# Kernel optimization log

Measured on AMD Instinct MI355X. Metric: run time of the kernel, lower is better.

## Reference

```python
import jax, jax.numpy as jnp
import numpy as np

# sizes / constants (mirroring the source module's constants)
M, T_SOL, NX, NY = 12, 64, 256, 256
N_TIMES, NOUT = 50, 256
LX, LY_TARGET = 60.0, 75.0
C_CU_TARGET, C_NI_TARGET = 0.001, 0.0001
T_MAX = 200.0
SIGMA, H, DH = 0.25, 4, 8


def setup_inputs() -> dict:
    key = jax.random.key(0)
    ks = jax.random.split(key, 7)
    u = jax.random.uniform(ks[0], (M, 3), dtype=jnp.float32)
    # rows: (Ly in [30,120], c_Cu in [0,0.0029], c_Ni in [0,0.0018])
    params = jnp.stack([30.0 + 90.0 * u[:, 0], 0.0029 * u[:, 1], 0.0018 * u[:, 2]], axis=1)
    c1_src = jax.random.uniform(ks[1], (M, T_SOL, NX, NY), dtype=jnp.float32) * 0.003
    c2_src = jax.random.uniform(ks[2], (M, T_SOL, NX, NY), dtype=jnp.float32) * 0.002
    Wq = jax.random.normal(ks[3], (H * DH, 3), dtype=jnp.float32) * 0.5
    bq = jax.random.normal(ks[4], (H * DH,), dtype=jnp.float32) * 0.1
    Wk = jax.random.normal(ks[5], (H * DH, 3), dtype=jnp.float32) * 0.5
    bk = jax.random.normal(ks[6], (H * DH,), dtype=jnp.float32) * 0.1
    return {"params": params, "c1_src": c1_src, "c2_src": c2_src,
            "Wq": Wq, "bq": bq, "Wk": Wk, "bk": bk}


def _bilinear_resample(xs, ys, vals, xq, yq):
    """RegularGridInterpolator(linear, fill_value=0) on grid (xs[NX], ys[NY]).
    vals: [T, NX, NY]; query is the outer-product grid xq[PX] x yq[PY].
    Separable bilinear -> [T, PX, PY]."""
    ix = jnp.clip(jnp.searchsorted(xs, xq, side='right') - 1, 0, xs.shape[0] - 2)
    tx = (xq - xs[ix]) / (xs[ix + 1] - xs[ix])
    vx = vals[:, ix, :] * (1.0 - tx)[None, :, None] + vals[:, ix + 1, :] * tx[None, :, None]
    iy = jnp.clip(jnp.searchsorted(ys, yq, side='right') - 1, 0, ys.shape[0] - 2)
    ty = (yq - ys[iy]) / (ys[iy + 1] - ys[iy])
    out = vx[:, :, iy] * (1.0 - ty)[None, None, :] + vx[:, :, iy + 1] * ty[None, None, :]
    inb = ((xq >= xs[0]) & (xq <= xs[-1]))[:, None] & ((yq >= ys[0]) & (yq <= ys[-1]))[None, :]
    return jnp.where(inb[None], out, jnp.float32(0.0))


def _forward(params, c1_src, c2_src, Wq, bq, Wk, bk):
    lys, c_cus, c_nis = params[:, 0], params[:, 1], params[:, 2]
    ly_n = (lys - 30.0) / 90.0
    ccu_n = c_cus / 0.0029
    cni_n = c_nis / 0.0018
    p = jnp.stack([ly_n, ccu_n, cni_n], axis=1)                      # [M,3]
    t = jnp.array([[(LY_TARGET - 30.0) / 90.0,
                    C_CU_TARGET / 0.0029,
                    C_NI_TARGET / 0.0018]], dtype=params.dtype)       # [1,3]
    Q = (t @ Wq.T + bq).reshape(1, H, DH)
    K = (p @ Wk.T + bk).reshape(-1, H, DH)
    attn = jnp.einsum('nhd,mhd->nmh', K, Q) / (DH ** 0.5)            # [M,1,H]
    attn_w = jax.nn.softmax(attn, axis=0).mean(axis=2)[:, 0]         # [M]
    dist2 = (((ly_n - t[0, 0]) / SIGMA) ** 2
             + ((ccu_n - t[0, 1]) / SIGMA) ** 2
             + ((cni_n - t[0, 2]) / SIGMA) ** 2)
    sw = jnp.exp(-dist2 / 2.0)
    sw = sw / sw.sum()
    w = attn_w * sw
    w = w / w.sum()                                                  # [M]

    # grids: source x shared; per-solution y grid rescaled to [0, LY_TARGET]
    xs = jnp.linspace(0.0, LX, NX)
    ys_scaled = (jnp.linspace(0.0, 1.0, NY)[None, :] * lys[:, None]) * (LY_TARGET / lys)[:, None]  # [M,NY]
    xq = jnp.linspace(0.0, LX, NOUT)
    yq = jnp.linspace(0.0, LY_TARGET, NOUT)

    times = jnp.linspace(0.0, min(T_MAX, T_MAX), N_TIMES)
    tidx = jnp.clip((times / T_MAX * T_SOL).astype(jnp.int32), 0, T_SOL - 1)  # [T]
    c1_sel = c1_src[:, tidx]                                          # [M,T,NX,NY]
    c2_sel = c2_src[:, tidx]

    res1, res2 = jax.vmap(
        lambda ys, v1, v2: (_bilinear_resample(xs, ys, v1, xq, yq),
                            _bilinear_resample(xs, ys, v2, xq, yq))
    )(ys_scaled, c1_sel, c2_sel)                                      # each [M,T,NOUT,NOUT]

    c1 = jnp.einsum('m,mtij->tij', w, res1)
    c2 = jnp.einsum('m,mtij->tij', w, res2)
    c1 = c1.at[:, :, 0].set(C_CU_TARGET)
    c2 = c2.at[:, :, -1].set(C_NI_TARGET)
    return jnp.stack([c1, c2])                                        # [2,T,NOUT,NOUT]


def reference(params, c1_src, c2_src, Wq, bq, Wk, bk):
    return _forward(params, c1_src, c2_src, Wq, bq, Wk, bk)
```

## Files before the change

kernel.cpp:

```cpp
#include <hip/hip_runtime.h>

#define MM    12
#define TSOL  64
#define NXX   256
#define NYY   256
#define NTT   50
#define NOUTT 256

__device__ float g_c[MM * NOUTT];
__device__ float g_w[MM];
__device__ float g_w255[MM];

__global__ __launch_bounds__(256) void ai_setup_kernel(
    const float* __restrict__ params,
    const float* __restrict__ Wq, const float* __restrict__ bq,
    const float* __restrict__ Wk, const float* __restrict__ bk)
{
    const int k = threadIdx.x;
    const int m = blockIdx.x;

    __shared__ float s_attn[MM][4];
    __shared__ float s_sw[MM];
    __shared__ float s_wm;
    __shared__ float s_ys[NYY];

    if (k < MM) {
        float ly = params[k * 3 + 0];
        float p0 = (ly - 30.0f) / 90.0f;
        float p1 = params[k * 3 + 1] / 0.0029f;
        float p2 = params[k * 3 + 2] / 0.0018f;
        const float t0 = 0.5f;
        const float t1 = 0.001f / 0.0029f;
        const float t2 = 0.0001f / 0.0018f;
        for (int h = 0; h < 4; ++h) {
            float acc = 0.0f;
            for (int d = 0; d < 8; ++d) {
                int o = h * 8 + d;
                float q  = t0 * Wq[o * 3 + 0] + t1 * Wq[o * 3 + 1] + t2 * Wq[o * 3 + 2] + bq[o];
                float kv = p0 * Wk[o * 3 + 0] + p1 * Wk[o * 3 + 1] + p2 * Wk[o * 3 + 2] + bk[o];
                acc += kv * q;
            }
            s_attn[k][h] = acc * 0.35355339059327373f;
        }
        float d0 = (p0 - t0) / 0.25f;
        float d1 = (p1 - t1) / 0.25f;
        float d2 = (p2 - t2) / 0.25f;
        s_sw[k] = expf(-(d0 * d0 + d1 * d1 + d2 * d2) * 0.5f);
    }
    __syncthreads();

    if (k == 0) {
        float aw[MM];
        for (int j = 0; j < MM; ++j) aw[j] = 0.0f;
        for (int h = 0; h < 4; ++h) {
            float mx = s_attn[0][h];
            for (int j = 1; j < MM; ++j) mx = fmaxf(mx, s_attn[j][h]);
            float e[MM]; float sum = 0.0f;
            for (int j = 0; j < MM; ++j) { e[j] = expf(s_attn[j][h] - mx); sum += e[j]; }
            for (int j = 0; j < MM; ++j) aw[j] += e[j] / sum;
        }
        float swsum = 0.0f;
        for (int j = 0; j < MM; ++j) swsum += s_sw[j];
        float wj[MM]; float wsum = 0.0f;
        for (int j = 0; j < MM; ++j) {
            wj[j] = (aw[j] * 0.25f) * (s_sw[j] / swsum);
            wsum += wj[j];
        }
        s_wm = wj[m] / wsum;
    }

    {
        float ly  = params[m * 3 + 0];
        float inv = 75.0f / ly;
        float l01 = (float)k * (1.0f / 255.0f);
        s_ys[k] = (l01 * ly) * inv;
    }
    __syncthreads();

    float w  = s_wm;
    float yq = (float)k * (75.0f / 255.0f);
    int l = 0, r = NYY;
    while (l < r) { int mid = (l + r) >> 1; if (s_ys[mid] <= yq) l = mid + 1; else r = mid; }
    int iy = l - 1;
    iy = iy < 0 ? 0 : (iy > NYY - 2 ? NYY - 2 : iy);
    float ty  = (yq - s_ys[iy]) / (s_ys[iy + 1] - s_ys[iy]);
    bool  inb = (yq >= s_ys[0]) && (yq <= s_ys[NYY - 1]);
    float a = inb ? w * (1.0f - ty) : 0.0f;
    float b = inb ? w * ty          : 0.0f;
    bool sel = (iy == k);
    g_c[m * NOUTT + k] = sel ? b : -a;
    if (k == 0)   g_w[m]    = w;
    if (k == 255) g_w255[m] = inb ? w : 0.0f;
}

__global__ __launch_bounds__(256) void ai_resample_kernel(
    const float* __restrict__ c1, const float* __restrict__ c2,
    float* __restrict__ out)
{
    __shared__ float s_c[MM * NOUTT];

    const int tid  = threadIdx.x;
    const int lane = tid & 63;
    const int wv   = tid >> 6;
    const int t    = blockIdx.y;
    const int i    = blockIdx.x * 4 + wv;
    int tsrc = (t * TSOL) / (NTT - 1);
    if (tsrc > TSOL - 1) tsrc = TSOL - 1;
    const int k0   = lane * 4;
    const bool l63 = (lane == 63);

#pragma unroll
    for (int c = 0; c < 3; ++c) {
        const float* gp = g_c + c * 1024 + wv * 256 + lane * 4;
        float*       lp = s_c + c * 1024 + wv * 256;
        __builtin_amdgcn_global_load_lds(
            (const __attribute__((address_space(1))) void*)gp,
            (__attribute__((address_space(3))) void*)lp, 16, 0, 0);
    }

    float wmv[MM], w2v[MM];
#pragma unroll
    for (int m = 0; m < MM; ++m) { wmv[m] = g_w[m]; w2v[m] = g_w255[m]; }

    const size_t rowoff = (size_t)tsrc * (NXX * NYY) + (size_t)i * NYY + (size_t)k0;

    float4 st[MM];
#pragma unroll
    for (int m = 0; m < MM; ++m)
        st[m] = *(const float4*)(c1 + (size_t)m * (TSOL * NXX * NYY) + rowoff);

    __syncthreads();

    float4 acc1 = {0.f, 0.f, 0.f, 0.f};
    float4 acc2 = {0.f, 0.f, 0.f, 0.f};

#pragma unroll
    for (int m = 0; m < MM; ++m) {
        float4 s = st[m];
        float lft = __shfl_up(s.w, 1);
        float rgt = __shfl_down(s.x, 1);
        float4 c  = *(const float4*)&s_c[m * NOUTT + k0];
        float wm_ = wmv[m];
        float w_w = l63 ? w2v[m] : wm_;
        acc1.x += wm_ * s.x + fabsf(c.x) * (((__float_as_int(c.x) >= 0) ? s.y : lft) - s.x);
        acc1.y += wm_ * s.y + fabsf(c.y) * (((__float_as_int(c.y) >= 0) ? s.z : s.x) - s.y);
        acc1.z += wm_ * s.z + fabsf(c.z) * (((__float_as_int(c.z) >= 0) ? s.w : s.y) - s.z);
        acc1.w += w_w * s.w + fabsf(c.w) * (((__float_as_int(c.w) >= 0) ? rgt : s.z) - s.w);
    }

#pragma unroll
    for (int m = 0; m < MM; ++m)
        st[m] = *(const float4*)(c2 + (size_t)m * (TSOL * NXX * NYY) + rowoff);
#pragma unroll
    for (int m = 0; m < MM; ++m) {
        float4 s = st[m];
        float lft = __shfl_up(s.w, 1);
        float rgt = __shfl_down(s.x, 1);
        float4 c  = *(const float4*)&s_c[m * NOUTT + k0];
        float wm_ = wmv[m];
        float w_w = l63 ? w2v[m] : wm_;
        acc2.x += wm_ * s.x + fabsf(c.x) * (((__float_as_int(c.x) >= 0) ? s.y : lft) - s.x);
        acc2.y += wm_ * s.y + fabsf(c.y) * (((__float_as_int(c.y) >= 0) ? s.z : s.x) - s.y);
        acc2.z += wm_ * s.z + fabsf(c.z) * (((__float_as_int(c.z) >= 0) ? s.w : s.y) - s.z);
        acc2.w += w_w * s.w + fabsf(c.w) * (((__float_as_int(c.w) >= 0) ? rgt : s.z) - s.w);
    }

    if (lane == 0) acc1.x = 0.001f;
    if (l63)       acc2.w = 0.0001f;

    *(float4*)&out[((size_t)t * NOUTT + (size_t)i) * NOUTT + (size_t)k0] = acc1;
    *(float4*)&out[((size_t)(NTT + t) * NOUTT + (size_t)i) * NOUTT + (size_t)k0] = acc2;
}

extern "C" void kernel_launch(void* const* d_in, const int* in_sizes, int n_in,
                              void* d_out, int out_size, void* d_ws, size_t ws_size,
                              hipStream_t stream) {
    const float* params = (const float*)d_in[0];
    const float* c1     = (const float*)d_in[1];
    const float* c2     = (const float*)d_in[2];
    const float* Wq     = (const float*)d_in[3];
    const float* bq     = (const float*)d_in[4];
    const float* Wk     = (const float*)d_in[5];
    const float* bk     = (const float*)d_in[6];
    float* out = (float*)d_out;

    ai_setup_kernel<<<dim3(MM), dim3(256), 0, stream>>>(params, Wq, bq, Wk, bk);
    ai_resample_kernel<<<dim3(NOUTT / 4, NTT), dim3(256), 0, stream>>>(c1, c2, out);
}
```

Measured before the change: 409.0 us.

## Process four rows per wave with double-buffered loads across solutions

Each wave now handles four output rows instead of one, and the grid shrinks accordingly. Loads for the next solution m+1 (both c1 and c2, four rows each) are issued before the current m is computed, in a two-stage register double buffer. The c1 and c2 accumulations are fused into one loop over m. The aim is to overlap memory latency with compute and reuse the per-m coefficients, at the cost of fewer blocks (800) and a launch-bounds occupancy hint that may limit register headroom.

```diff
diff --git a/kernel.cpp b/kernel.cpp
--- a/kernel.cpp
+++ b/kernel.cpp
@@ -6,6 +6,8 @@
 #define NYY   256
 #define NTT   50
 #define NOUTT 256
+#define ICH   16
+#define RPW   4
 
 __device__ float g_c[MM * NOUTT];
 __device__ float g_w[MM];
@@ -93,7 +95,7 @@
     if (k == 255) g_w255[m] = inb ? w : 0.0f;
 }
 
-__global__ __launch_bounds__(256) void ai_resample_kernel(
+__global__ __launch_bounds__(256, 3) void ai_resample_kernel(
     const float* __restrict__ c1, const float* __restrict__ c2,
     float* __restrict__ out)
 {
@@ -103,9 +105,9 @@
     const int lane = tid & 63;
     const int wv   = tid >> 6;
     const int t    = blockIdx.y;
-    const int i    = blockIdx.x * 4 + wv;
     int tsrc = (t * TSOL) / (NTT - 1);
     if (tsrc > TSOL - 1) tsrc = TSOL - 1;
+    const int i0   = blockIdx.x * ICH + wv * RPW;
     const int k0   = lane * 4;
     const bool l63 = (lane == 63);
 
@@ -122,54 +124,71 @@
 #pragma unroll
     for (int m = 0; m < MM; ++m) { wmv[m] = g_w[m]; w2v[m] = g_w255[m]; }
 
-    const size_t rowoff = (size_t)tsrc * (NXX * NYY) + (size_t)i * NYY + (size_t)k0;
-
-    float4 st[MM];
-#pragma unroll
-    for (int m = 0; m < MM; ++m)
-        st[m] = *(const float4*)(c1 + (size_t)m * (TSOL * NXX * NYY) + rowoff);
+    const size_t SLAB = (size_t)TSOL * NXX * NYY;
+    const size_t roff = (size_t)tsrc * (NXX * NYY) + (size_t)i0 * NYY + (size_t)k0;
+
+    float4 sA[2][RPW], sB[2][RPW];
+
+#pragma unroll
+    for (int r = 0; r < RPW; ++r)
+        sA[0][r] = *(const float4*)(c1 + roff + (size_t)r * NYY);
+#pragma unroll
+    for (int r = 0; r < RPW; ++r)
+        sB[0][r] = *(const float4*)(c2 + roff + (size_t)r * NYY);
 
     __syncthreads();
 
-    float4 acc1 = {0.f, 0.f, 0.f, 0.f};
-    float4 acc2 = {0.f, 0.f, 0.f, 0.f};
+    float4 acc1[RPW], acc2[RPW];
+#pragma unroll
+    for (int r = 0; r < RPW; ++r) {
+        acc1[r] = make_float4(0.f, 0.f, 0.f, 0.f);
+        acc2[r] = make_float4(0.f, 0.f, 0.f, 0.f);
+    }
 
 #pragma unroll
     for (int m = 0; m < MM; ++m) {
-        float4 s = st[m];
-        float lft = __shfl_up(s.w, 1);
-        float rgt = __shfl_down(s.x, 1);
-        float4 c  = *(const float4*)&s_c[m * NOUTT + k0];
-        float wm_ = wmv[m];
-        float w_w = l63 ? w2v[m] : wm_;
-        acc1.x += wm_ * s.x + fabsf(c.x) * (((__float_as_int(c.x) >= 0) ? s.y : lft) - s.x);
-        acc1.y += wm_ * s.y + fabsf(c.y) * (((__float_as_int(c.y) >= 0) ? s.z : s.x) - s.y);
-        acc1.z += wm_ * s.z + fabsf(c.z) * (((__float_as_int(c.z) >= 0) ? s.w : s.y) - s.z);
-        acc1.w += w_w * s.w + fabsf(c.w) * (((__float_as_int(c.w) >= 0) ? rgt : s.z) - s.w);
-    }
-
-#pragma unroll
-    for (int m = 0; m < MM; ++m)
-        st[m] = *(const float4*)(c2 + (size_t)m * (TSOL * NXX * NYY) + rowoff);
-#pragma unroll
-    for (int m = 0; m < MM; ++m) {
-        float4 s = st[m];
-        float lft = __shfl_up(s.w, 1);
-        float rgt = __shfl_down(s.x, 1);
-        float4 c  = *(const float4*)&s_c[m * NOUTT + k0];
-        float wm_ = wmv[m];
-        float w_w = l63 ? w2v[m] : wm_;
-        acc2.x += wm_ * s.x + fabsf(c.x) * (((__float_as_int(c.x) >= 0) ? s.y : lft) - s.x);
-        acc2.y += wm_ * s.y + fabsf(c.y) * (((__float_as_int(c.y) >= 0) ? s.z : s.x) - s.y);
-        acc2.z += wm_ * s.z + fabsf(c.z) * (((__float_as_int(c.z) >= 0) ? s.w : s.y) - s.z);
-        acc2.w += w_w * s.w + fabsf(c.w) * (((__float_as_int(c.w) >= 0) ? rgt : s.z) - s.w);
-    }
-
-    if (lane == 0) acc1.x = 0.001f;
-    if (l63)       acc2.w = 0.0001f;
-
-    *(float4*)&out[((size_t)t * NOUTT + (size_t)i) * NOUTT + (size_t)k0] = acc1;
-    *(float4*)&out[((size_t)(NTT + t) * NOUTT + (size_t)i) * NOUTT + (size_t)k0] = acc2;
+        const int cur = m & 1;
+        const int nxt = cur ^ 1;
+        if (m < MM - 1) {
+            const size_t b = (size_t)(m + 1) * SLAB + roff;
+#pragma unroll
+            for (int r = 0; r < RPW; ++r)
+                sA[nxt][r] = *(const float4*)(c1 + b + (size_t)r * NYY);
+#pragma unroll
+            for (int r = 0; r < RPW; ++r)
+                sB[nxt][r] = *(const float4*)(c2 + b + (size_t)r * NYY);
+        }
+        const float4 cc  = *(const float4*)&s_c[m * NOUTT + k0];
+        const float  wm_ = wmv[m];
+        const float  w_w = l63 ? w2v[m] : wm_;
+#pragma unroll
+        for (int r = 0; r < RPW; ++r) {
+            float4 s = sA[cur][r];
+            float lft = __shfl_up(s.w, 1);
+            float rgt = __shfl_down(s.x, 1);
+            acc1[r].x += wm_ * s.x + fabsf(cc.x) * (((__float_as_int(cc.x) >= 0) ? s.y : lft) - s.x);
+            acc1[r].y += wm_ * s.y + fabsf(cc.y) * (((__float_as_int(cc.y) >= 0) ? s.z : s.x) - s.y);
+            acc1[r].z += wm_ * s.z + fabsf(cc.z) * (((__float_as_int(cc.z) >= 0) ? s.w : s.y) - s.z);
+            acc1[r].w += w_w * s.w + fabsf(cc.w) * (((__float_as_int(cc.w) >= 0) ? rgt : s.z) - s.w);
+            s = sB[cur][r];
+            lft = __shfl_up(s.w, 1);
+            rgt = __shfl_down(s.x, 1);
+            acc2[r].x += wm_ * s.x + fabsf(cc.x) * (((__float_as_int(cc.x) >= 0) ? s.y : lft) - s.x);
+            acc2[r].y += wm_ * s.y + fabsf(cc.y) * (((__float_as_int(cc.y) >= 0) ? s.z : s.x) - s.y);
+            acc2[r].z += wm_ * s.z + fabsf(cc.z) * (((__float_as_int(cc.z) >= 0) ? s.w : s.y) - s.z);
+            acc2[r].w += w_w * s.w + fabsf(cc.w) * (((__float_as_int(cc.w) >= 0) ? rgt : s.z) - s.w);
+        }
+    }
+
+#pragma unroll
+    for (int r = 0; r < RPW; ++r) {
+        const int i = i0 + r;
+        float4 a1 = acc1[r], a2 = acc2[r];
+        if (lane == 0) a1.x = 0.001f;
+        if (l63)       a2.w = 0.0001f;
+        *(float4*)&out[((size_t)t * NOUTT + (size_t)i) * NOUTT + (size_t)k0] = a1;
+        *(float4*)&out[((size_t)(NTT + t) * NOUTT + (size_t)i) * NOUTT + (size_t)k0] = a2;
+    }
 }
 
 extern "C" void kernel_launch(void* const* d_in, const int* in_sizes, int n_in,
@@ -185,5 +204,5 @@
     float* out = (float*)d_out;
 
     ai_setup_kernel<<<dim3(MM), dim3(256), 0, stream>>>(params, Wq, bq, Wk, bk);
-    ai_resample_kernel<<<dim3(NOUTT / 4, NTT), dim3(256), 0, stream>>>(c1, c2, out);
+    ai_resample_kernel<<<dim3(NOUTT / ICH, NTT), dim3(256), 0, stream>>>(c1, c2, out);
 }
```

Result: slower. 592.2 us (+44.8%).
